# Kernel optimization log

Measured on AMD Instinct MI355X. Metric: run time of the kernel, lower is better.

The kernel has to match this reference:

```python
import jax, jax.numpy as jnp
import numpy as np

N_NODES = 100000
N_EDGES = 1600000
IN_DIM = 128
OUT_DIM = 64


def setup_inputs() -> dict:
    key = jax.random.key(0)
    k1, k2, k3, k4, k5 = jax.random.split(key, 5)
    return {
        "h_init": jax.random.normal(k1, (N_NODES, IN_DIM), dtype=jnp.float32),
        "W1": jax.random.normal(k2, (OUT_DIM, IN_DIM), dtype=jnp.float32),
        "a": jax.random.normal(k3, (1, OUT_DIM), dtype=jnp.float32),
        "src": jax.random.randint(k4, (N_EDGES,), 0, N_NODES, dtype=jnp.int64)
        if jax.config.jax_enable_x64 else jax.random.randint(k4, (N_EDGES,), 0, N_NODES, dtype=jnp.int32),
        "dst": jax.random.randint(k5, (N_EDGES,), 0, N_NODES, dtype=jnp.int32),
    }


def reference(h_init, W1, a, src, dst):
    N = h_init.shape[0]
    # node projection: [N, out_dim]
    h = h_init @ W1.T
    # per-edge diff feature: dst minus src (DGL edges.dst['h'] - edges.src['h'])
    diff = h[dst] - h[src]                       # [E, out_dim]
    e = jnp.tanh(diff @ a[0])                    # [E] edge attention logit
    # segment softmax over incoming edges of each destination node
    seg_max = jax.ops.segment_max(e, dst, num_segments=N)   # [N]
    ex = jnp.exp(e - seg_max[dst])               # [E]
    denom = jax.ops.segment_sum(ex, dst, num_segments=N)    # [N]
    alpha = ex / denom[dst]                      # [E]
    # weighted sum of diff features per destination node
    h_diff = jax.ops.segment_sum(alpha[:, None] * diff, dst, num_segments=N)  # [N, out_dim]
    return jax.nn.relu(h + h_diff)
```

## Files before the change

kernel.cpp:

```cpp
#include <hip/hip_runtime.h>
#include <hip/hip_fp16.h>

#define N_NODES 100000
#define N_EDGES 1600000
#define IN_DIM 128
#define OUT_DIM 64

#define NBUCK 391
#define BIN_NBLK 800
#define BIN_CHUNK 2000
#define MAXB 4608

#define PROJ_BLKS 1563
#define SORT_THREADS 1024

typedef short short8 __attribute__((ext_vector_type(8)));
typedef float f32x4 __attribute__((ext_vector_type(4)));

__device__ __forceinline__ short bf16_trunc(float x) {
  return (short)(__float_as_uint(x) >> 16);
}
__device__ __forceinline__ float bf16_tof(short s) {
  return __uint_as_float(((unsigned)(unsigned short)s) << 16);
}
__device__ __forceinline__ float edge_ex(float p) {
  float t2 = __expf(2.f * p);
  float th = 1.f - 2.f * __builtin_amdgcn_rcpf(t2 + 1.f);
  return __expf(th);
}

__global__ __launch_bounds__(256) void fat1_kernel(
    const float* __restrict__ h_init, const float* __restrict__ W1,
    const float* __restrict__ a, const int* __restrict__ src,
    const int* __restrict__ dst, float* __restrict__ h,
    __half* __restrict__ h16, float* __restrict__ ha,
    int* __restrict__ bucket_cursor, unsigned int* __restrict__ pairs) {
  __shared__ __align__(16) char smem[16 * 64 * 8 * 2 * sizeof(short)];

  if (blockIdx.x < BIN_NBLK) {
    int* hst = (int*)smem;
    int* cur = hst + NBUCK;
    for (int i = threadIdx.x; i < NBUCK; i += 256) hst[i] = 0;
    __syncthreads();
    int beg = blockIdx.x * BIN_CHUNK;
    int end = min(beg + BIN_CHUNK, N_EDGES);
    for (int e = beg + threadIdx.x; e < end; e += 256)
      atomicAdd(&hst[dst[e] >> 8], 1);
    __syncthreads();
    for (int i = threadIdx.x; i < NBUCK; i += 256) {
      int c = hst[i];
      cur[i] = (c > 0) ? atomicAdd(&bucket_cursor[i], c) + i * MAXB : 0;
    }
    __syncthreads();
    for (int e = beg + threadIdx.x; e < end; e += 256) {
      int d = dst[e];
      int pos = atomicAdd(&cur[d >> 8], 1);
      pairs[pos] = ((unsigned int)src[e] << 8) | (unsigned int)(d & 255);
    }
    return;
  }

  int pb = blockIdx.x - BIN_NBLK;
  short* whi = (short*)smem;
  short* wlo = whi + 16 * 64 * 8;

  for (int idx = threadIdx.x; idx < 16 * 64; idx += 256) {
    int f = idx >> 6;
    int l = idx & 63;
    int kc = f >> 2, ot = f & 3;
    const float* wsrc =
        W1 + (ot * 16 + (l & 15)) * IN_DIM + kc * 32 + (l >> 4) * 8;
    short hi[8], lo[8];
#pragma unroll
    for (int j = 0; j < 8; j++) {
      float x = wsrc[j];
      short hv = bf16_trunc(x);
      hi[j] = hv;
      lo[j] = bf16_trunc(x - bf16_tof(hv));
    }
    *(short8*)&whi[idx * 8] = *(const short8*)hi;
    *(short8*)&wlo[idx * 8] = *(const short8*)lo;
  }

  int row0 = pb * 64;
  int w = threadIdx.x >> 6;
  int l = threadIdx.x & 63;
  int m = l & 15;
  int q = l >> 4;

  int arow = row0 + w * 16 + m;
  if (arow >= N_NODES) arow = N_NODES - 1;
  const float* xsrc = h_init + (size_t)arow * IN_DIM + q * 8;

  short8 ahi[4], alo[4];
#pragma unroll
  for (int kc = 0; kc < 4; kc++) {
    float xv[8];
    *(float4*)&xv[0] = *(const float4*)(xsrc + kc * 32);
    *(float4*)&xv[4] = *(const float4*)(xsrc + kc * 32 + 4);
    short hi[8], lo[8];
#pragma unroll
    for (int j = 0; j < 8; j++) {
      short hv = bf16_trunc(xv[j]);
      hi[j] = hv;
      lo[j] = bf16_trunc(xv[j] - bf16_tof(hv));
    }
    ahi[kc] = *(const short8*)hi;
    alo[kc] = *(const short8*)lo;
  }
  __syncthreads();

  f32x4 acc[4] = {{0.f, 0.f, 0.f, 0.f},
                  {0.f, 0.f, 0.f, 0.f},
                  {0.f, 0.f, 0.f, 0.f},
                  {0.f, 0.f, 0.f, 0.f}};

#pragma unroll
  for (int kc = 0; kc < 4; kc++) {
#pragma unroll
    for (int ot = 0; ot < 4; ot++) {
      int base = (((kc << 2) | ot) * 64 + l) * 8;
      short8 bhi = *(const short8*)&whi[base];
      short8 blo = *(const short8*)&wlo[base];
      acc[ot] = __builtin_amdgcn_mfma_f32_16x16x32_bf16(ahi[kc], bhi, acc[ot],
                                                        0, 0, 0);
      acc[ot] = __builtin_amdgcn_mfma_f32_16x16x32_bf16(ahi[kc], blo, acc[ot],
                                                        0, 0, 0);
      acc[ot] = __builtin_amdgcn_mfma_f32_16x16x32_bf16(alo[kc], bhi, acc[ot],
                                                        0, 0, 0);
    }
  }

  float pa[4] = {0.f, 0.f, 0.f, 0.f};
#pragma unroll
  for (int ot = 0; ot < 4; ot++) {
    float aval = a[ot * 16 + m];
#pragma unroll
    for (int r = 0; r < 4; r++) pa[r] += acc[ot][r] * aval;
  }
  int rowb = row0 + w * 16 + q * 4;
#pragma unroll
  for (int r = 0; r < 4; r++) {
    int row = rowb + r;
    if (row < N_NODES) {
#pragma unroll
      for (int ot = 0; ot < 4; ot++) {
        h[(size_t)row * OUT_DIM + ot * 16 + m] = acc[ot][r];
        h16[(size_t)row * OUT_DIM + ot * 16 + m] = __float2half(acc[ot][r]);
      }
    }
  }
#pragma unroll
  for (int r = 0; r < 4; r++) {
    pa[r] += __shfl_xor(pa[r], 1);
    pa[r] += __shfl_xor(pa[r], 2);
    pa[r] += __shfl_xor(pa[r], 4);
    pa[r] += __shfl_xor(pa[r], 8);
  }
  if (m == 0) {
#pragma unroll
    for (int r = 0; r < 4; r++) {
      int row = rowb + r;
      if (row < N_NODES) ha[row] = pa[r];
    }
  }
}

__global__ __launch_bounds__(SORT_THREADS) void bucket_sort_kernel(
    const unsigned int* __restrict__ pairs,
    const int* __restrict__ bucket_cursor, const float* __restrict__ ha,
    int* __restrict__ nbeg, int* __restrict__ nend, int2* __restrict__ sorted) {
  __shared__ unsigned int plds[MAXB];
  __shared__ int hist[256];
  __shared__ int excl[256];
  __shared__ float had[256];
  int b = blockIdx.x;
  int t = threadIdx.x;
  int pbeg = b * MAXB;
  int cnt = bucket_cursor[b];

  if (t < 256) {
    int node = (b << 8) + t;
    had[t] = (node < N_NODES) ? ha[node] : 0.f;
    hist[t] = 0;
  }
  __syncthreads();

  for (int i = t; i < cnt; i += SORT_THREADS) {
    unsigned int p = pairs[pbeg + i];
    plds[i] = p;
    atomicAdd(&hist[p & 255u], 1);
  }
  __syncthreads();

  int v = 0;
  if (t < 256) {
    v = hist[t];
    excl[t] = v;
  }
  __syncthreads();
  for (int off = 1; off < 256; off <<= 1) {
    int u = (t >= off && t < 256) ? excl[t - off] : 0;
    __syncthreads();
    if (t < 256) excl[t] += u;
    __syncthreads();
  }
  if (t < 256) {
    int my_excl = excl[t] - v;
    int node = (b << 8) + t;
    if (node < N_NODES) {
      nbeg[node] = pbeg + my_excl;
      nend[node] = pbeg + my_excl + v;
    }
    hist[t] = my_excl;
  }
  __syncthreads();

  for (int i = t; i < cnt; i += SORT_THREADS) {
    unsigned int p = plds[i];
    int d = (int)(p & 255u);
    int s = (int)(p >> 8);
    int pos = atomicAdd(&hist[d], 1);
    float ex = edge_ex(had[d] - ha[s]);
    sorted[pbeg + pos] = make_int2(s << 7, __float_as_int(ex));
  }
}

__global__ __launch_bounds__(256) void gather_kernel(
    const float* __restrict__ h, const __half* __restrict__ h16,
    const int* __restrict__ nbeg, const int* __restrict__ nend,
    const int2* __restrict__ sorted, float* __restrict__ out) {
  int wave = (blockIdx.x * 256 + threadIdx.x) >> 6;
  int lane = threadIdx.x & 63;
  if (wave >= N_NODES) return;
  int n = wave;
  int beg = nbeg[n];
  int end = nend[n];
  int g = lane >> 3;
  int l8 = lane & 7;

  const float4* h4 = (const float4*)h;
  float4 hd0 = h4[(size_t)n * (OUT_DIM / 4) + l8 * 2];
  float4 hd1 = h4[(size_t)n * (OUT_DIM / 4) + l8 * 2 + 1];

  const char* h16b = (const char*)h16;
  float acc[8] = {0.f, 0.f, 0.f, 0.f, 0.f, 0.f, 0.f, 0.f};
  float den = 0.f;

  for (int base = beg + g * 4; base < end; base += 32) {
    int last = end - 1;
    int2 e[4];
    float exv[4];
#pragma unroll
    for (int k = 0; k < 4; k++) {
      int i = base + k;
      e[k] = sorted[i < end ? i : last];
      exv[k] = (i < end) ? __int_as_float(e[k].y) : 0.f;
    }
    uint4 uv[4];
#pragma unroll
    for (int k = 0; k < 4; k++)
      uv[k] = *(const uint4*)(h16b + e[k].x + (l8 << 4));
#pragma unroll
    for (int k = 0; k < 4; k++) {
      union {
        uint4 u;
        __half hh[8];
      } U;
      U.u = uv[k];
      float ex = exv[k];
      den += ex;
#pragma unroll
      for (int j = 0; j < 8; j++)
        acc[j] = fmaf(__half2float(U.hh[j]), ex, acc[j]);
    }
  }

#pragma unroll
  for (int j = 0; j < 8; j++) {
    acc[j] += __shfl_xor(acc[j], 8);
    acc[j] += __shfl_xor(acc[j], 16);
    acc[j] += __shfl_xor(acc[j], 32);
  }
  den += __shfl_xor(den, 8);
  den += __shfl_xor(den, 16);
  den += __shfl_xor(den, 32);

  if (g == 0) {
    bool has = den > 0.f;
    float inv = has ? __builtin_amdgcn_rcpf(den) : 0.f;
    float4 r0, r1;
    r0.x = fmaxf(has ? 2.f * hd0.x - acc[0] * inv : hd0.x, 0.f);
    r0.y = fmaxf(has ? 2.f * hd0.y - acc[1] * inv : hd0.y, 0.f);
    r0.z = fmaxf(has ? 2.f * hd0.z - acc[2] * inv : hd0.z, 0.f);
    r0.w = fmaxf(has ? 2.f * hd0.w - acc[3] * inv : hd0.w, 0.f);
    r1.x = fmaxf(has ? 2.f * hd1.x - acc[4] * inv : hd1.x, 0.f);
    r1.y = fmaxf(has ? 2.f * hd1.y - acc[5] * inv : hd1.y, 0.f);
    r1.z = fmaxf(has ? 2.f * hd1.z - acc[6] * inv : hd1.z, 0.f);
    r1.w = fmaxf(has ? 2.f * hd1.w - acc[7] * inv : hd1.w, 0.f);
    float4* o4 = (float4*)out;
    o4[(size_t)n * (OUT_DIM / 4) + l8 * 2] = r0;
    o4[(size_t)n * (OUT_DIM / 4) + l8 * 2 + 1] = r1;
  }
}

extern "C" void kernel_launch(void* const* d_in, const int* in_sizes, int n_in,
                              void* d_out, int out_size, void* d_ws,
                              size_t ws_size, hipStream_t stream) {
  const float* h_init = (const float*)d_in[0];
  const float* W1 = (const float*)d_in[1];
  const float* a = (const float*)d_in[2];
  const int* src = (const int*)d_in[3];
  const int* dst = (const int*)d_in[4];
  float* out = (float*)d_out;

  float* h = (float*)d_ws;
  __half* h16 = (__half*)(h + (size_t)N_NODES * OUT_DIM);
  float* ha = (float*)(h16 + (size_t)N_NODES * OUT_DIM);
  unsigned int* pairs = (unsigned int*)(ha + N_NODES);
  int2* sorted = (int2*)(pairs + (size_t)NBUCK * MAXB);
  int* nbeg = (int*)(sorted + (size_t)NBUCK * MAXB);
  int* nend = nbeg + N_NODES;
  int* bucket_cursor = nend + N_NODES;

  hipMemsetAsync(bucket_cursor, 0, NBUCK * sizeof(int), stream);
  fat1_kernel<<<BIN_NBLK + PROJ_BLKS, 256, 0, stream>>>(
      h_init, W1, a, src, dst, h, h16, ha, bucket_cursor, pairs);
  bucket_sort_kernel<<<NBUCK, SORT_THREADS, 0, stream>>>(
      pairs, bucket_cursor, ha, nbeg, nend, sorted);
  gather_kernel<<<(N_NODES * 64 + 255) / 256, 256, 0, stream>>>(
      h, h16, nbeg, nend, sorted, out);
}
```

Before: 203.1 us.

## Fuse bucket sort with gather in LDS and interleave binning with projection blocks

Merges the bucket sort and gather kernels into one kernel. Each 1024-thread block sorts its bucket's edges into LDS and then gathers features for its 256 destination nodes straight from LDS, so the sorted edge array and the node begin/end arrays no longer go through global memory. The binning blocks are cut to 250 larger chunks and spread one in every seven blocks among the projection blocks, and each bucket cursor is padded to its own stride to reduce atomic contention. The trade-off is that only 391 large blocks now do the gather, with heavy LDS use (about 55KB), which may cut occupancy and load balance compared with the old one-wave-per-node launch.

```diff
diff --git a/kernel.cpp b/kernel.cpp
--- a/kernel.cpp
+++ b/kernel.cpp
@@ -7,12 +7,16 @@
 #define OUT_DIM 64
 
 #define NBUCK 391
-#define BIN_NBLK 800
-#define BIN_CHUNK 2000
 #define MAXB 4608
+#define CUR_STRIDE 16
+
+#define BIN_NBLK 250
+#define BIN_CHUNK 6400
 
 #define PROJ_BLKS 1563
-#define SORT_THREADS 1024
+#define PB_GRID (PROJ_BLKS + BIN_NBLK)
+
+#define SG_THREADS 1024
 
 typedef short short8 __attribute__((ext_vector_type(8)));
 typedef float f32x4 __attribute__((ext_vector_type(4)));
@@ -29,7 +33,7 @@
   return __expf(th);
 }
 
-__global__ __launch_bounds__(256) void fat1_kernel(
+__global__ __launch_bounds__(256) void fused_pb_kernel(
     const float* __restrict__ h_init, const float* __restrict__ W1,
     const float* __restrict__ a, const int* __restrict__ src,
     const int* __restrict__ dst, float* __restrict__ h,
@@ -37,19 +41,22 @@
     int* __restrict__ bucket_cursor, unsigned int* __restrict__ pairs) {
   __shared__ __align__(16) char smem[16 * 64 * 8 * 2 * sizeof(short)];
 
-  if (blockIdx.x < BIN_NBLK) {
+  int idx = blockIdx.x;
+  int q7 = idx / 7, r7 = idx % 7;
+  if (r7 == 3 && q7 < BIN_NBLK) {
     int* hst = (int*)smem;
     int* cur = hst + NBUCK;
     for (int i = threadIdx.x; i < NBUCK; i += 256) hst[i] = 0;
     __syncthreads();
-    int beg = blockIdx.x * BIN_CHUNK;
-    int end = min(beg + BIN_CHUNK, N_EDGES);
+    int beg = q7 * BIN_CHUNK;
+    int end = beg + BIN_CHUNK;
     for (int e = beg + threadIdx.x; e < end; e += 256)
       atomicAdd(&hst[dst[e] >> 8], 1);
     __syncthreads();
     for (int i = threadIdx.x; i < NBUCK; i += 256) {
       int c = hst[i];
-      cur[i] = (c > 0) ? atomicAdd(&bucket_cursor[i], c) + i * MAXB : 0;
+      cur[i] = (c > 0) ? atomicAdd(&bucket_cursor[i * CUR_STRIDE], c) + i * MAXB
+                       : 0;
     }
     __syncthreads();
     for (int e = beg + threadIdx.x; e < end; e += 256) {
@@ -60,13 +67,13 @@
     return;
   }
 
-  int pb = blockIdx.x - BIN_NBLK;
+  int pb = idx - min(q7 + (r7 > 3 ? 1 : 0), BIN_NBLK);
   short* whi = (short*)smem;
   short* wlo = whi + 16 * 64 * 8;
 
-  for (int idx = threadIdx.x; idx < 16 * 64; idx += 256) {
-    int f = idx >> 6;
-    int l = idx & 63;
+  for (int i2 = threadIdx.x; i2 < 16 * 64; i2 += 256) {
+    int f = i2 >> 6;
+    int l = i2 & 63;
     int kc = f >> 2, ot = f & 3;
     const float* wsrc =
         W1 + (ot * 16 + (l & 15)) * IN_DIM + kc * 32 + (l >> 4) * 8;
@@ -78,8 +85,8 @@
       hi[j] = hv;
       lo[j] = bf16_trunc(x - bf16_tof(hv));
     }
-    *(short8*)&whi[idx * 8] = *(const short8*)hi;
-    *(short8*)&wlo[idx * 8] = *(const short8*)lo;
+    *(short8*)&whi[i2 * 8] = *(const short8*)hi;
+    *(short8*)&wlo[i2 * 8] = *(const short8*)lo;
   }
 
   int row0 = pb * 64;
@@ -166,141 +173,126 @@
   }
 }
 
-__global__ __launch_bounds__(SORT_THREADS) void bucket_sort_kernel(
-    const unsigned int* __restrict__ pairs,
-    const int* __restrict__ bucket_cursor, const float* __restrict__ ha,
-    int* __restrict__ nbeg, int* __restrict__ nend, int2* __restrict__ sorted) {
+__global__ __launch_bounds__(SG_THREADS) void sortgather_kernel(
+    const float* __restrict__ h, const __half* __restrict__ h16,
+    const float* __restrict__ ha, const int* __restrict__ bucket_cursor,
+    const unsigned int* __restrict__ pairs, float* __restrict__ out) {
   __shared__ unsigned int plds[MAXB];
+  __shared__ int2 slds[MAXB];
+  __shared__ float had[256];
   __shared__ int hist[256];
-  __shared__ int excl[256];
-  __shared__ float had[256];
+  __shared__ int scn[256];
+  __shared__ int cur[256];
   int b = blockIdx.x;
   int t = threadIdx.x;
-  int pbeg = b * MAXB;
-  int cnt = bucket_cursor[b];
+  int node0 = b << 8;
+  int cnt = min(bucket_cursor[b * CUR_STRIDE], MAXB);
 
   if (t < 256) {
-    int node = (b << 8) + t;
+    int node = node0 + t;
     had[t] = (node < N_NODES) ? ha[node] : 0.f;
     hist[t] = 0;
   }
   __syncthreads();
-
-  for (int i = t; i < cnt; i += SORT_THREADS) {
-    unsigned int p = pairs[pbeg + i];
+  for (int i = t; i < cnt; i += SG_THREADS) {
+    unsigned int p = pairs[(size_t)b * MAXB + i];
     plds[i] = p;
     atomicAdd(&hist[p & 255u], 1);
   }
   __syncthreads();
-
-  int v = 0;
-  if (t < 256) {
-    v = hist[t];
-    excl[t] = v;
-  }
+  int v = (t < 256) ? hist[t] : 0;
+  if (t < 256) scn[t] = v;
   __syncthreads();
   for (int off = 1; off < 256; off <<= 1) {
-    int u = (t >= off && t < 256) ? excl[t - off] : 0;
-    __syncthreads();
-    if (t < 256) excl[t] += u;
-    __syncthreads();
-  }
-  if (t < 256) {
-    int my_excl = excl[t] - v;
-    int node = (b << 8) + t;
-    if (node < N_NODES) {
-      nbeg[node] = pbeg + my_excl;
-      nend[node] = pbeg + my_excl + v;
-    }
-    hist[t] = my_excl;
-  }
-  __syncthreads();
-
-  for (int i = t; i < cnt; i += SORT_THREADS) {
+    int u = (t >= off && t < 256) ? scn[t - off] : 0;
+    __syncthreads();
+    if (t < 256) scn[t] += u;
+    __syncthreads();
+  }
+  if (t < 256) cur[t] = scn[t] - v;
+  __syncthreads();
+  for (int i = t; i < cnt; i += SG_THREADS) {
     unsigned int p = plds[i];
-    int d = (int)(p & 255u);
+    int nl = (int)(p & 255u);
     int s = (int)(p >> 8);
-    int pos = atomicAdd(&hist[d], 1);
-    float ex = edge_ex(had[d] - ha[s]);
-    sorted[pbeg + pos] = make_int2(s << 7, __float_as_int(ex));
-  }
-}
-
-__global__ __launch_bounds__(256) void gather_kernel(
-    const float* __restrict__ h, const __half* __restrict__ h16,
-    const int* __restrict__ nbeg, const int* __restrict__ nend,
-    const int2* __restrict__ sorted, float* __restrict__ out) {
-  int wave = (blockIdx.x * 256 + threadIdx.x) >> 6;
-  int lane = threadIdx.x & 63;
-  if (wave >= N_NODES) return;
-  int n = wave;
-  int beg = nbeg[n];
-  int end = nend[n];
+    float ex = edge_ex(had[nl] - ha[s]);
+    int pos = atomicAdd(&cur[nl], 1);
+    slds[pos] = make_int2(s << 7, __float_as_int(ex));
+  }
+  __syncthreads();
+
+  int wv = t >> 6;
+  int lane = t & 63;
   int g = lane >> 3;
   int l8 = lane & 7;
-
+  const char* h16b = (const char*)h16;
   const float4* h4 = (const float4*)h;
-  float4 hd0 = h4[(size_t)n * (OUT_DIM / 4) + l8 * 2];
-  float4 hd1 = h4[(size_t)n * (OUT_DIM / 4) + l8 * 2 + 1];
-
-  const char* h16b = (const char*)h16;
-  float acc[8] = {0.f, 0.f, 0.f, 0.f, 0.f, 0.f, 0.f, 0.f};
-  float den = 0.f;
-
-  for (int base = beg + g * 4; base < end; base += 32) {
-    int last = end - 1;
-    int2 e[4];
-    float exv[4];
-#pragma unroll
-    for (int k = 0; k < 4; k++) {
-      int i = base + k;
-      e[k] = sorted[i < end ? i : last];
-      exv[k] = (i < end) ? __int_as_float(e[k].y) : 0.f;
-    }
-    uint4 uv[4];
-#pragma unroll
-    for (int k = 0; k < 4; k++)
-      uv[k] = *(const uint4*)(h16b + e[k].x + (l8 << 4));
-#pragma unroll
-    for (int k = 0; k < 4; k++) {
-      union {
-        uint4 u;
-        __half hh[8];
-      } U;
-      U.u = uv[k];
-      float ex = exv[k];
-      den += ex;
-#pragma unroll
-      for (int j = 0; j < 8; j++)
-        acc[j] = fmaf(__half2float(U.hh[j]), ex, acc[j]);
-    }
-  }
-
-#pragma unroll
-  for (int j = 0; j < 8; j++) {
-    acc[j] += __shfl_xor(acc[j], 8);
-    acc[j] += __shfl_xor(acc[j], 16);
-    acc[j] += __shfl_xor(acc[j], 32);
-  }
-  den += __shfl_xor(den, 8);
-  den += __shfl_xor(den, 16);
-  den += __shfl_xor(den, 32);
-
-  if (g == 0) {
-    bool has = den > 0.f;
-    float inv = has ? __builtin_amdgcn_rcpf(den) : 0.f;
-    float4 r0, r1;
-    r0.x = fmaxf(has ? 2.f * hd0.x - acc[0] * inv : hd0.x, 0.f);
-    r0.y = fmaxf(has ? 2.f * hd0.y - acc[1] * inv : hd0.y, 0.f);
-    r0.z = fmaxf(has ? 2.f * hd0.z - acc[2] * inv : hd0.z, 0.f);
-    r0.w = fmaxf(has ? 2.f * hd0.w - acc[3] * inv : hd0.w, 0.f);
-    r1.x = fmaxf(has ? 2.f * hd1.x - acc[4] * inv : hd1.x, 0.f);
-    r1.y = fmaxf(has ? 2.f * hd1.y - acc[5] * inv : hd1.y, 0.f);
-    r1.z = fmaxf(has ? 2.f * hd1.z - acc[6] * inv : hd1.z, 0.f);
-    r1.w = fmaxf(has ? 2.f * hd1.w - acc[7] * inv : hd1.w, 0.f);
-    float4* o4 = (float4*)out;
-    o4[(size_t)n * (OUT_DIM / 4) + l8 * 2] = r0;
-    o4[(size_t)n * (OUT_DIM / 4) + l8 * 2 + 1] = r1;
+  float4* o4 = (float4*)out;
+
+  for (int nl = wv; nl < 256; nl += 16) {
+    int node = node0 + nl;
+    if (node >= N_NODES) break;
+    int endp = scn[nl];
+    int begp = endp - hist[nl];
+    float4 hd0 = h4[(size_t)node * (OUT_DIM / 4) + l8 * 2];
+    float4 hd1 = h4[(size_t)node * (OUT_DIM / 4) + l8 * 2 + 1];
+    float acc[8] = {0.f, 0.f, 0.f, 0.f, 0.f, 0.f, 0.f, 0.f};
+    float den = 0.f;
+    int last = endp - 1;
+
+    for (int base = begp + g * 4; base < endp; base += 32) {
+      int2 e[4];
+      float exv[4];
+#pragma unroll
+      for (int k = 0; k < 4; k++) {
+        int i = base + k;
+        e[k] = slds[i < endp ? i : last];
+        exv[k] = (i < endp) ? __int_as_float(e[k].y) : 0.f;
+      }
+      uint4 uv[4];
+#pragma unroll
+      for (int k = 0; k < 4; k++)
+        uv[k] = *(const uint4*)(h16b + e[k].x + (l8 << 4));
+#pragma unroll
+      for (int k = 0; k < 4; k++) {
+        union {
+          uint4 u;
+          __half hh[8];
+        } U;
+        U.u = uv[k];
+        float ex = exv[k];
+        den += ex;
+#pragma unroll
+        for (int j = 0; j < 8; j++)
+          acc[j] = fmaf(__half2float(U.hh[j]), ex, acc[j]);
+      }
+    }
+
+#pragma unroll
+    for (int j = 0; j < 8; j++) {
+      acc[j] += __shfl_xor(acc[j], 8);
+      acc[j] += __shfl_xor(acc[j], 16);
+      acc[j] += __shfl_xor(acc[j], 32);
+    }
+    den += __shfl_xor(den, 8);
+    den += __shfl_xor(den, 16);
+    den += __shfl_xor(den, 32);
+
+    if (g == 0) {
+      bool has = den > 0.f;
+      float inv = has ? __builtin_amdgcn_rcpf(den) : 0.f;
+      float4 r0, r1;
+      r0.x = fmaxf(has ? 2.f * hd0.x - acc[0] * inv : hd0.x, 0.f);
+      r0.y = fmaxf(has ? 2.f * hd0.y - acc[1] * inv : hd0.y, 0.f);
+      r0.z = fmaxf(has ? 2.f * hd0.z - acc[2] * inv : hd0.z, 0.f);
+      r0.w = fmaxf(has ? 2.f * hd0.w - acc[3] * inv : hd0.w, 0.f);
+      r1.x = fmaxf(has ? 2.f * hd1.x - acc[4] * inv : hd1.x, 0.f);
+      r1.y = fmaxf(has ? 2.f * hd1.y - acc[5] * inv : hd1.y, 0.f);
+      r1.z = fmaxf(has ? 2.f * hd1.z - acc[6] * inv : hd1.z, 0.f);
+      r1.w = fmaxf(has ? 2.f * hd1.w - acc[7] * inv : hd1.w, 0.f);
+      o4[(size_t)node * (OUT_DIM / 4) + l8 * 2] = r0;
+      o4[(size_t)node * (OUT_DIM / 4) + l8 * 2 + 1] = r1;
+    }
   }
 }
 
@@ -318,16 +310,11 @@
   __half* h16 = (__half*)(h + (size_t)N_NODES * OUT_DIM);
   float* ha = (float*)(h16 + (size_t)N_NODES * OUT_DIM);
   unsigned int* pairs = (unsigned int*)(ha + N_NODES);
-  int2* sorted = (int2*)(pairs + (size_t)NBUCK * MAXB);
-  int* nbeg = (int*)(sorted + (size_t)NBUCK * MAXB);
-  int* nend = nbeg + N_NODES;
-  int* bucket_cursor = nend + N_NODES;
-
-  hipMemsetAsync(bucket_cursor, 0, NBUCK * sizeof(int), stream);
-  fat1_kernel<<<BIN_NBLK + PROJ_BLKS, 256, 0, stream>>>(
-      h_init, W1, a, src, dst, h, h16, ha, bucket_cursor, pairs);
-  bucket_sort_kernel<<<NBUCK, SORT_THREADS, 0, stream>>>(
-      pairs, bucket_cursor, ha, nbeg, nend, sorted);
-  gather_kernel<<<(N_NODES * 64 + 255) / 256, 256, 0, stream>>>(
-      h, h16, nbeg, nend, sorted, out);
-}
+  int* bucket_cursor = (int*)(pairs + (size_t)NBUCK * MAXB);
+
+  hipMemsetAsync(bucket_cursor, 0, NBUCK * CUR_STRIDE * sizeof(int), stream);
+  fused_pb_kernel<<<PB_GRID, 256, 0, stream>>>(h_init, W1, a, src, dst, h, h16,
+                                               ha, bucket_cursor, pairs);
+  sortgather_kernel<<<NBUCK, SG_THREADS, 0, stream>>>(h, h16, ha, bucket_cursor,
+                                                      pairs, out);
+}
```

New measurement: 214.9 us. +5.9%, slower.
